# Kernel tuning notes

Hardware: AMD Instinct MI355X
Metric: run time of the kernel (lower is better)

The kernel has to match this reference:

```python
import jax, jax.numpy as jnp
import numpy as np

N_HEADS = 16
SEG = 64
EPS = 1e-6


def _sigma(x):
    # ELU(x) + 1 kernel feature map (strictly positive)
    return jax.nn.elu(x) + 1.0


def setup_inputs() -> dict:
    key = jax.random.key(0)
    kx, kq, kk, kv, ko = jax.random.split(key, 5)
    B, T, D = 4, 4096, 1024
    scale = D ** -0.5
    return {
        "x": jax.random.normal(kx, (B, T, D), dtype=jnp.float32),
        "W_q": jax.random.normal(kq, (D, D), dtype=jnp.float32) * scale,
        "W_k": jax.random.normal(kk, (D, D), dtype=jnp.float32) * scale,
        "W_v": jax.random.normal(kv, (D, D), dtype=jnp.float32) * scale,
        "W_o": jax.random.normal(ko, (D, D), dtype=jnp.float32) * scale,
        "beta_param": jnp.zeros((N_HEADS,), dtype=jnp.float32),
    }


def _infini_attention(x, W_q, W_k, W_v, W_o, beta_param):
    B, T, D = x.shape
    H = N_HEADS
    dk = D // H
    assert T % SEG == 0
    S = T // SEG

    def proj(W):
        # nn.Linear: x @ W.T ; split heads -> (B,H,T,dk) -> (S,B,H,SEG,dk)
        y = (x @ W.T).reshape(B, T, H, dk).transpose(0, 2, 1, 3)
        return y.reshape(B, H, S, SEG, dk).transpose(2, 0, 1, 3, 4)

    Qs, Ks, Vs = proj(W_q), proj(W_k), proj(W_v)

    beta = jax.nn.sigmoid(beta_param).reshape(1, H, 1, 1)
    causal = jnp.triu(jnp.ones((SEG, SEG), dtype=bool), k=1)
    inv_sqrt_dk = 1.0 / jnp.sqrt(jnp.asarray(dk, x.dtype))

    M0 = jnp.zeros((B, H, dk, dk), dtype=x.dtype)
    z0 = jnp.zeros((B, H, dk), dtype=x.dtype)

    def step(carry, qkv):
        M, z = carry
        q, k, v = qkv  # each (B,H,SEG,dk)
        # Eq.4 memory retrieval
        sq = _sigma(q)
        denom_q = jnp.sum(sq * z[:, :, None, :], axis=-1, keepdims=True) + EPS
        A_mem = jnp.matmul(sq, M) / denom_q
        # local causal softmax attention
        scores = jnp.matmul(q, jnp.swapaxes(k, -2, -1)) * inv_sqrt_dk
        scores = jnp.where(causal, -jnp.inf, scores)
        A_dot = jnp.matmul(jax.nn.softmax(scores, axis=-1), v)
        A_s = beta * A_mem + (1.0 - beta) * A_dot
        # Eq.5 delta-rule memory update
        sk = _sigma(k)
        denom_k = jnp.sum(sk * z[:, :, None, :], axis=-1, keepdims=True) + EPS
        V_prev = jnp.matmul(sk, M) / denom_k
        M_new = M + jnp.einsum("bhtk,bhtv->bhkv", sk, v - V_prev)
        z_new = z + jnp.sum(sk, axis=-2)
        return (M_new, z_new), A_s

    (M, z), outs = jax.lax.scan(step, (M0, z0), (Qs, Ks, Vs))
    # outs: (S,B,H,SEG,dk) -> (B,T,D)
    out = outs.transpose(1, 3, 0, 2, 4).reshape(B, S * SEG, H, dk)
    # careful: need segment-major time ordering -> (B, H, T, dk) then (B,T,H,dk)
    out = outs.transpose(1, 2, 0, 3, 4).reshape(B, H, T, dk)
    out = out.transpose(0, 2, 1, 3).reshape(B, T, D)
    out = out @ W_o.T
    return out, M.mean(0), z.mean(0)


def reference(x, W_q, W_k, W_v, W_o, beta_param):
    return _infini_attention(x, W_q, W_k, W_v, W_o, beta_param)
```

## Files before the change

kernel.cpp:

```cpp
#include <hip/hip_runtime.h>

typedef __bf16 bf16_t;
typedef __bf16 bf16x8 __attribute__((ext_vector_type(8)));
typedef __bf16 bf16x4 __attribute__((ext_vector_type(4)));
typedef float  f32x4  __attribute__((ext_vector_type(4)));

__device__ __forceinline__ void gload16(const bf16_t* g, bf16_t* l) {
    __builtin_amdgcn_global_load_lds(
        (const __attribute__((address_space(1))) void*)(g),
        (__attribute__((address_space(3))) void*)(l), 16, 0, 0);
}

__global__ __launch_bounds__(256) void cast_bf16_kernel(const float* __restrict__ in,
                                                        bf16_t* __restrict__ out, int n4) {
    int i = blockIdx.x * 256 + threadIdx.x;
    if (i >= n4) return;
    f32x4 v = *reinterpret_cast<const f32x4*>(in + (size_t)i * 4);
    bf16x4 o;
    o[0] = (bf16_t)v[0]; o[1] = (bf16_t)v[1]; o[2] = (bf16_t)v[2]; o[3] = (bf16_t)v[3];
    *reinterpret_cast<bf16x4*>(out + (size_t)i * 4) = o;
}

__device__ __forceinline__ bf16x8 sigma8(bf16x8 x) {
    bf16x8 o;
#pragma unroll
    for (int j = 0; j < 8; j++) {
        float f = (float)x[j];
        float sg = f > 0.f ? f + 1.f : __expf(f);
        o[j] = (bf16_t)sg;
    }
    return o;
}

template <int OUT_BF16>
__global__ __launch_bounds__(512, 2) void gemm256(const bf16_t* __restrict__ A,
                                                  const bf16_t* __restrict__ Bm,
                                                  void* __restrict__ Cv,
                                                  int M, int N, int K) {
    __shared__ bf16_t As[4][256 * 32];
    __shared__ bf16_t Bs[4][256 * 32];

    int bid = blockIdx.x;
    int xq = bid & 7, jq = bid >> 3;
    int bm = xq * 8 + (jq >> 2), bn = jq & 3;

    int tid = threadIdx.x;
    int w = tid >> 6, lane = tid & 63;
    int wm = w >> 2, wn = w & 3;
    int lr = lane & 15, lk = lane >> 4;

    int srow = lane >> 2;
    int schunk = (lane & 3) ^ (srow & 3);
    const bf16_t* gA0 = A  + (size_t)(bm * 256 + w * 32 + srow) * K + schunk * 8;
    const bf16_t* gA1 = gA0 + (size_t)16 * K;
    const bf16_t* gB0 = Bm + (size_t)(bn * 256 + w * 32 + srow) * K + schunk * 8;
    const bf16_t* gB1 = gB0 + (size_t)16 * K;
    int lO0 = (w * 32) * 32 + lane * 8;
    int lO1 = (w * 32 + 16) * 32 + lane * 8;

    int chunkb = (lk ^ (lr & 3)) << 4;
    int aoff[8], boff[4];
#pragma unroll
    for (int mi = 0; mi < 8; mi++) aoff[mi] = (wm * 128 + mi * 16 + lr) * 64 + chunkb;
#pragma unroll
    for (int ni = 0; ni < 4; ni++) boff[ni] = (wn * 64 + ni * 16 + lr) * 64 + chunkb;

    f32x4 acc[8][4];
#pragma unroll
    for (int mi = 0; mi < 8; mi++)
#pragma unroll
        for (int ni = 0; ni < 4; ni++) acc[mi][ni] = (f32x4){0.f, 0.f, 0.f, 0.f};

    const int NT = K >> 5;

    auto STAGE = [&](int t) {
        int slot = t & 3;
        size_t ko = (size_t)t * 32;
        gload16(gA0 + ko, &As[slot][lO0]);
        gload16(gA1 + ko, &As[slot][lO1]);
        gload16(gB0 + ko, &Bs[slot][lO0]);
        gload16(gB1 + ko, &Bs[slot][lO1]);
    };

    STAGE(0); STAGE(1); STAGE(2);

#pragma unroll 1
    for (int t = 0; t < NT; ++t) {
        int ahead = NT - 1 - t;
        if (ahead >= 2)      asm volatile("s_waitcnt vmcnt(8)" ::: "memory");
        else if (ahead == 1) asm volatile("s_waitcnt vmcnt(4)" ::: "memory");
        else                 asm volatile("s_waitcnt vmcnt(0)" ::: "memory");
        __builtin_amdgcn_sched_barrier(0);
        __builtin_amdgcn_s_barrier();
        __builtin_amdgcn_sched_barrier(0);

        const char* pa = (const char*)(&As[t & 3][0]);
        const char* pb = (const char*)(&Bs[t & 3][0]);
        bf16x8 af[8], bfr[4];
#pragma unroll
        for (int mi = 0; mi < 8; mi++)
            af[mi] = *reinterpret_cast<const bf16x8*>(pa + aoff[mi]);
#pragma unroll
        for (int ni = 0; ni < 4; ni++)
            bfr[ni] = *reinterpret_cast<const bf16x8*>(pb + boff[ni]);

        if (t + 3 < NT) STAGE(t + 3);

        asm volatile("s_waitcnt lgkmcnt(0)" ::: "memory");
        __builtin_amdgcn_sched_barrier(0);
        __builtin_amdgcn_s_setprio(1);
#pragma unroll
        for (int mi = 0; mi < 8; mi++)
#pragma unroll
            for (int ni = 0; ni < 4; ni++)
                acc[mi][ni] = __builtin_amdgcn_mfma_f32_16x16x32_bf16(af[mi], bfr[ni], acc[mi][ni], 0, 0, 0);
        __builtin_amdgcn_s_setprio(0);
    }

    int row0 = bm * 256 + wm * 128 + lk * 4;
    int col0 = bn * 256 + wn * 64 + lr;
#pragma unroll
    for (int mi = 0; mi < 8; mi++)
#pragma unroll
        for (int ni = 0; ni < 4; ni++)
#pragma unroll
            for (int jj = 0; jj < 4; jj++) {
                size_t idx = (size_t)(row0 + mi * 16 + jj) * N + (col0 + ni * 16);
                float v = acc[mi][ni][jj];
                if (OUT_BF16) reinterpret_cast<bf16_t*>(Cv)[idx] = (bf16_t)v;
                else          reinterpret_cast<float*>(Cv)[idx]  = v;
            }
}

__global__ __launch_bounds__(256) void attn_kernel(const bf16_t* __restrict__ Qb,
                                                   bf16_t* __restrict__ Kb,
                                                   bf16_t* __restrict__ Vb,
                                                   bf16_t* __restrict__ skTg,
                                                   float* __restrict__ csum,
                                                   bf16_t* __restrict__ Adot) {
    __shared__ bf16_t kS[64 * 72];
    __shared__ bf16_t vS[64 * 72];
    __shared__ bf16_t skT[64 * 72];
    __shared__ bf16_t vT[64 * 72];
    __shared__ bf16_t pS[64 * 72];
    __shared__ float  scr[64 * 68];

    int u = blockIdx.x;
    int bh = u >> 6, s = u & 63;
    int b = bh >> 4, h = bh & 15;
    int tid = threadIdx.x;
    int w = tid >> 6, lane = tid & 63;
    int lr = lane & 15, lk = lane >> 4;
    int r = tid >> 2, qd = tid & 3, c0 = qd << 4;

    size_t vseg = ((size_t)b * 4096 + s * 64) * 1024 + (size_t)h * 64;
    size_t sb = ((size_t)bh * 64 + s) * 4096;

    {
        bf16x8 k0 = *reinterpret_cast<const bf16x8*>(Kb + vseg + (size_t)r * 1024 + c0);
        bf16x8 k1 = *reinterpret_cast<const bf16x8*>(Kb + vseg + (size_t)r * 1024 + c0 + 8);
        bf16x8 v0 = *reinterpret_cast<const bf16x8*>(Vb + vseg + (size_t)r * 1024 + c0);
        bf16x8 v1 = *reinterpret_cast<const bf16x8*>(Vb + vseg + (size_t)r * 1024 + c0 + 8);
        *reinterpret_cast<bf16x8*>(&kS[r * 72 + c0])     = k0;
        *reinterpret_cast<bf16x8*>(&kS[r * 72 + c0 + 8]) = k1;
        *reinterpret_cast<bf16x8*>(&vS[r * 72 + c0])     = v0;
        *reinterpret_cast<bf16x8*>(&vS[r * 72 + c0 + 8]) = v1;
        bf16x8 s0 = sigma8(k0), s1 = sigma8(k1);
        *reinterpret_cast<bf16x8*>(Kb + vseg + (size_t)r * 1024 + c0)     = s0;
        *reinterpret_cast<bf16x8*>(Kb + vseg + (size_t)r * 1024 + c0 + 8) = s1;
#pragma unroll
        for (int j = 0; j < 8; j++) {
            skT[(c0 + j) * 72 + r]     = s0[j];
            skT[(c0 + 8 + j) * 72 + r] = s1[j];
            vT[(c0 + j) * 72 + r]      = v0[j];
            vT[(c0 + 8 + j) * 72 + r]  = v1[j];
        }
    }
    __syncthreads();

    if (tid < 64) {
        float acc = 0.f;
#pragma unroll 8
        for (int t = 0; t < 64; t++) acc += (float)skT[tid * 72 + t];
        csum[((size_t)bh * 64 + s) * 64 + tid] = acc;
    }
    *reinterpret_cast<bf16x8*>(skTg + sb + (size_t)r * 64 + c0) =
        *reinterpret_cast<const bf16x8*>(&skT[r * 72 + c0]);
    *reinterpret_cast<bf16x8*>(skTg + sb + (size_t)r * 64 + c0 + 8) =
        *reinterpret_cast<const bf16x8*>(&skT[r * 72 + c0 + 8]);
    *reinterpret_cast<bf16x8*>(Vb + vseg + (size_t)r * 1024 + c0) =
        *reinterpret_cast<const bf16x8*>(&vT[r * 72 + c0]);
    *reinterpret_cast<bf16x8*>(Vb + vseg + (size_t)r * 1024 + c0 + 8) =
        *reinterpret_cast<const bf16x8*>(&vT[r * 72 + c0 + 8]);

    {
        bf16x8 aq[2];
#pragma unroll
        for (int ks = 0; ks < 2; ks++)
            aq[ks] = *reinterpret_cast<const bf16x8*>(Qb + vseg + (size_t)(w * 16 + lr) * 1024 + lk * 8 + ks * 32);
        f32x4 sc[4];
#pragma unroll
        for (int ct = 0; ct < 4; ct++) {
            sc[ct] = (f32x4){0.f, 0.f, 0.f, 0.f};
#pragma unroll
            for (int ks = 0; ks < 2; ks++) {
                bf16x8 bfrag = *reinterpret_cast<const bf16x8*>(&kS[(ct * 16 + lr) * 72 + lk * 8 + ks * 32]);
                sc[ct] = __builtin_amdgcn_mfma_f32_16x16x32_bf16(aq[ks], bfrag, sc[ct], 0, 0, 0);
            }
        }
#pragma unroll
        for (int ct = 0; ct < 4; ct++)
#pragma unroll
            for (int j = 0; j < 4; j++)
                scr[(w * 16 + lk * 4 + j) * 68 + ct * 16 + lr] = sc[ct][j] * 0.125f;
    }
    __syncthreads();

    {
        float p[16];
        float mx = -3.4e38f;
        const float* srow_p = &scr[r * 68 + c0];
#pragma unroll
        for (int i = 0; i < 16; i++) {
            int c = c0 + i;
            float v = (c <= r) ? srow_p[i] : -3.4e38f;
            p[i] = v;
            mx = fmaxf(mx, v);
        }
        mx = fmaxf(mx, __shfl_xor(mx, 1));
        mx = fmaxf(mx, __shfl_xor(mx, 2));
        float sum = 0.f;
#pragma unroll
        for (int i = 0; i < 16; i++) {
            int c = c0 + i;
            float e = (c <= r) ? __expf(p[i] - mx) : 0.f;
            p[i] = e;
            sum += e;
        }
        sum += __shfl_xor(sum, 1);
        sum += __shfl_xor(sum, 2);
        float inv = 1.f / sum;
        bf16x8 p0, p1;
#pragma unroll
        for (int j = 0; j < 8; j++) {
            p0[j] = (bf16_t)(p[j] * inv);
            p1[j] = (bf16_t)(p[8 + j] * inv);
        }
        *reinterpret_cast<bf16x8*>(&pS[r * 72 + c0])     = p0;
        *reinterpret_cast<bf16x8*>(&pS[r * 72 + c0 + 8]) = p1;
    }
    __syncthreads();

    {
        f32x4 ad[4];
#pragma unroll
        for (int ct = 0; ct < 4; ct++) {
            ad[ct] = (f32x4){0.f, 0.f, 0.f, 0.f};
#pragma unroll
            for (int ks = 0; ks < 2; ks++) {
                bf16x8 afrag = *reinterpret_cast<const bf16x8*>(&pS[(w * 16 + lr) * 72 + lk * 8 + ks * 32]);
                bf16x8 bfrag = *reinterpret_cast<const bf16x8*>(&vT[(ct * 16 + lr) * 72 + lk * 8 + ks * 32]);
                ad[ct] = __builtin_amdgcn_mfma_f32_16x16x32_bf16(afrag, bfrag, ad[ct], 0, 0, 0);
            }
        }
#pragma unroll
        for (int ct = 0; ct < 4; ct++)
#pragma unroll
            for (int j = 0; j < 4; j++)
                kS[(w * 16 + lk * 4 + j) * 72 + ct * 16 + lr] = (bf16_t)ad[ct][j];
    }
    __syncthreads();
    *reinterpret_cast<bf16x8*>(Adot + sb + (size_t)r * 64 + c0) =
        *reinterpret_cast<const bf16x8*>(&kS[r * 72 + c0]);
    *reinterpret_cast<bf16x8*>(Adot + sb + (size_t)r * 64 + c0 + 8) =
        *reinterpret_cast<const bf16x8*>(&kS[r * 72 + c0 + 8]);
}

__global__ __launch_bounds__(64) void zprefix_kernel(const float* __restrict__ csum,
                                                     float* __restrict__ zx,
                                                     float* __restrict__ zfin) {
    int bh = blockIdx.x;
    int d = threadIdx.x;
    float z = 0.f;
    for (int s = 0; s < 64; s++) {
        size_t o = ((size_t)bh * 64 + s) * 64 + d;
        zx[o] = z;
        z += csum[o];
    }
    zfin[bh * 64 + d] = z;
}

__global__ __launch_bounds__(128) void denom_kernel(const bf16_t* __restrict__ Qb,
                                                    const bf16_t* __restrict__ sK,
                                                    const float* __restrict__ zx,
                                                    float* __restrict__ invq,
                                                    float* __restrict__ invk) {
    __shared__ float zL[64];
    int u = blockIdx.x;
    int bh = u >> 6, s = u & 63;
    int b = bh >> 4, h = bh & 15;
    int tid = threadIdx.x;
    if (tid < 64) zL[tid] = zx[((size_t)bh * 64 + s) * 64 + tid];
    __syncthreads();
    int row = tid & 63;
    bool isq = tid < 64;
    const bf16_t* src = (isq ? Qb : sK) +
                        ((size_t)b * 4096 + s * 64 + row) * 1024 + (size_t)h * 64;
    float acc = 0.f;
#pragma unroll
    for (int blk = 0; blk < 8; blk++) {
        bf16x8 v = *reinterpret_cast<const bf16x8*>(src + blk * 8);
#pragma unroll
        for (int j = 0; j < 8; j++) {
            float f = (float)v[j];
            float sg;
            if (isq) {
                sg = f > 0.f ? f + 1.f : __expf(f);
                sg = (float)(bf16_t)sg;
            } else {
                sg = f;
            }
            acc = __builtin_fmaf(sg, zL[blk * 8 + j], acc);
        }
    }
    float inv = 1.f / (acc + 1e-6f);
    float* dst = isq ? invq : invk;
    dst[((size_t)bh * 64 + s) * 64 + row] = inv;
}

__global__ __launch_bounds__(64, 1) void scan_kernel(const bf16_t* __restrict__ sK,
                                                     const bf16_t* __restrict__ vTg,
                                                     const bf16_t* __restrict__ skTg,
                                                     const float* __restrict__ invk,
                                                     bf16_t* __restrict__ Msnap,
                                                     float* __restrict__ Mfin) {
    __shared__ bf16_t MbL[16 * 72];
    __shared__ bf16_t uTL[16 * 72];
    __shared__ float  ikL[64];

    int blk = blockIdx.x;
    int bh = blk & 63, cq = blk >> 6;
    int c0 = cq << 4;
    int b = bh >> 4, h = bh & 15;
    int lane = threadIdx.x;
    int lr = lane & 15, lk = lane >> 4;
    int vr = lane >> 2, vt0 = (lane & 3) << 4;

    size_t chbase = ((size_t)b * 4096) * 1024 + (size_t)h * 64;
    size_t stbase = (size_t)bh * 64 * 4096;

    auto swz = [](bf16_t* base, int row, int intra) -> bf16_t* {
        return (bf16_t*)((char*)base + row * 144 + (intra ^ ((row & 7) << 4)));
    };

    for (int i = lane; i < 16 * 72; i += 64) MbL[i] = (bf16_t)0.f;
    f32x4 Mreg[4];
#pragma unroll
    for (int rt = 0; rt < 4; rt++) Mreg[rt] = (f32x4){0.f, 0.f, 0.f, 0.f};

    bf16x8 cK[4][2], cT[4][2];
#pragma unroll
    for (int rt = 0; rt < 4; rt++)
#pragma unroll
        for (int ks = 0; ks < 2; ks++) {
            cK[rt][ks] = *reinterpret_cast<const bf16x8*>(
                sK + chbase + (size_t)(rt * 16 + lr) * 1024 + lk * 8 + ks * 32);
            cT[rt][ks] = *reinterpret_cast<const bf16x8*>(
                skTg + stbase + (size_t)(rt * 16 + lr) * 64 + lk * 8 + ks * 32);
        }
    {
        bf16x8 v0 = *reinterpret_cast<const bf16x8*>(vTg + chbase + (size_t)(c0 + vr) * 1024 + vt0);
        bf16x8 v1 = *reinterpret_cast<const bf16x8*>(vTg + chbase + (size_t)(c0 + vr) * 1024 + vt0 + 8);
        *reinterpret_cast<bf16x8*>(swz(uTL, vr, vt0 * 2))      = v0;
        *reinterpret_cast<bf16x8*>(swz(uTL, vr, vt0 * 2 + 16)) = v1;
        ikL[lane] = invk[(size_t)bh * 4096 + lane];
    }

    for (int s = 0; s < 64; s++) {
        bf16x8 nK[4][2], nT[4][2], nv0, nv1;
        float nik = 0.f;
        if (s < 63) {
            size_t vs2 = chbase + (size_t)(s + 1) * 65536;
            size_t sb2 = stbase + (size_t)(s + 1) * 4096;
#pragma unroll
            for (int rt = 0; rt < 4; rt++)
#pragma unroll
                for (int ks = 0; ks < 2; ks++) {
                    nK[rt][ks] = *reinterpret_cast<const bf16x8*>(
                        sK + vs2 + (size_t)(rt * 16 + lr) * 1024 + lk * 8 + ks * 32);
                    nT[rt][ks] = *reinterpret_cast<const bf16x8*>(
                        skTg + sb2 + (size_t)(rt * 16 + lr) * 64 + lk * 8 + ks * 32);
                }
            nv0 = *reinterpret_cast<const bf16x8*>(vTg + vs2 + (size_t)(c0 + vr) * 1024 + vt0);
            nv1 = *reinterpret_cast<const bf16x8*>(vTg + vs2 + (size_t)(c0 + vr) * 1024 + vt0 + 8);
            nik = invk[(size_t)bh * 4096 + (size_t)(s + 1) * 64 + lane];
        }

        bf16x8 mb0 = *reinterpret_cast<const bf16x8*>(swz(MbL, lr, lk * 16));
        bf16x8 mb1 = *reinterpret_cast<const bf16x8*>(swz(MbL, lr, lk * 16 + 64));
        f32x4 Y[4];
#pragma unroll
        for (int rt = 0; rt < 4; rt++) {
            Y[rt] = (f32x4){0.f, 0.f, 0.f, 0.f};
            Y[rt] = __builtin_amdgcn_mfma_f32_16x16x32_bf16(cK[rt][0], mb0, Y[rt], 0, 0, 0);
            Y[rt] = __builtin_amdgcn_mfma_f32_16x16x32_bf16(cK[rt][1], mb1, Y[rt], 0, 0, 0);
        }

#pragma unroll
        for (int rt = 0; rt < 4; rt++) {
            bf16x4 vv = *reinterpret_cast<const bf16x4*>(swz(uTL, lr, rt * 32 + lk * 8));
            bf16x4 uu;
#pragma unroll
            for (int j = 0; j < 4; j++) {
                float ik = ikL[rt * 16 + lk * 4 + j];
                uu[j] = (bf16_t)((float)vv[j] - Y[rt][j] * ik);
            }
            *reinterpret_cast<bf16x4*>(swz(uTL, lr, rt * 32 + lk * 8)) = uu;
        }

        bf16x8 ub0 = *reinterpret_cast<const bf16x8*>(swz(uTL, lr, lk * 16));
        bf16x8 ub1 = *reinterpret_cast<const bf16x8*>(swz(uTL, lr, lk * 16 + 64));
#pragma unroll
        for (int rt = 0; rt < 4; rt++) {
            Mreg[rt] = __builtin_amdgcn_mfma_f32_16x16x32_bf16(cT[rt][0], ub0, Mreg[rt], 0, 0, 0);
            Mreg[rt] = __builtin_amdgcn_mfma_f32_16x16x32_bf16(cT[rt][1], ub1, Mreg[rt], 0, 0, 0);
        }

#pragma unroll
        for (int rt = 0; rt < 4; rt++) {
            bf16x4 mp;
#pragma unroll
            for (int j = 0; j < 4; j++) mp[j] = (bf16_t)Mreg[rt][j];
            *reinterpret_cast<bf16x4*>(swz(MbL, lr, rt * 32 + lk * 8)) = mp;
            if (s < 63)
                *reinterpret_cast<bf16x4*>(
                    Msnap + (((size_t)bh * 64 + s + 1) * 64 + c0 + lr) * 64 + rt * 16 + lk * 4) = mp;
        }

        if (s < 63) {
#pragma unroll
            for (int rt = 0; rt < 4; rt++)
#pragma unroll
                for (int ks = 0; ks < 2; ks++) { cK[rt][ks] = nK[rt][ks]; cT[rt][ks] = nT[rt][ks]; }
            *reinterpret_cast<bf16x8*>(swz(uTL, vr, vt0 * 2))      = nv0;
            *reinterpret_cast<bf16x8*>(swz(uTL, vr, vt0 * 2 + 16)) = nv1;
            ikL[lane] = nik;
        }
    }

#pragma unroll
    for (int rt = 0; rt < 4; rt++)
#pragma unroll
        for (int j = 0; j < 4; j++)
            Mfin[(size_t)bh * 4096 + (size_t)(rt * 16 + lk * 4 + j) * 64 + c0 + lr] = Mreg[rt][j];
}

__global__ __launch_bounds__(256) void combine_kernel(const bf16_t* __restrict__ Qb,
                                                      const bf16_t* __restrict__ Msnap,
                                                      const bf16_t* __restrict__ Adot,
                                                      const float* __restrict__ invq,
                                                      const float* __restrict__ beta_param,
                                                      bf16_t* __restrict__ Op) {
    __shared__ bf16_t oS[64 * 72];
    __shared__ bf16_t adS[64 * 72];
    __shared__ float  iq[64];

    int u = blockIdx.x;
    int bh = u >> 6, s = u & 63;
    int b = bh >> 4, h = bh & 15;
    int tid = threadIdx.x;
    int w = tid >> 6, lane = tid & 63;
    int lr = lane & 15, lk = lane >> 4;
    int r = tid >> 2, c0 = (tid & 3) << 4;

    size_t vseg = ((size_t)b * 4096 + s * 64) * 1024 + (size_t)h * 64;
    size_t sb = ((size_t)bh * 64 + s) * 4096;
    size_t ib = ((size_t)bh * 64 + s) * 64;

    float beta = 1.f / (1.f + __expf(-beta_param[h]));
    float omb = 1.f - beta;

    *reinterpret_cast<bf16x8*>(&adS[r * 72 + c0]) =
        *reinterpret_cast<const bf16x8*>(Adot + sb + (size_t)r * 64 + c0);
    *reinterpret_cast<bf16x8*>(&adS[r * 72 + c0 + 8]) =
        *reinterpret_cast<const bf16x8*>(Adot + sb + (size_t)r * 64 + c0 + 8);
    if (tid < 64) iq[tid] = invq[ib + tid];

    f32x4 Y[4];
#pragma unroll
    for (int ct = 0; ct < 4; ct++) Y[ct] = (f32x4){0.f, 0.f, 0.f, 0.f};
    if (s > 0) {
        bf16x8 aq[2];
#pragma unroll
        for (int ks = 0; ks < 2; ks++)
            aq[ks] = sigma8(*reinterpret_cast<const bf16x8*>(
                Qb + vseg + (size_t)(w * 16 + lr) * 1024 + lk * 8 + ks * 32));
#pragma unroll
        for (int ct = 0; ct < 4; ct++)
#pragma unroll
            for (int ks = 0; ks < 2; ks++) {
                bf16x8 bfrag = *reinterpret_cast<const bf16x8*>(
                    Msnap + sb + (size_t)(ct * 16 + lr) * 64 + lk * 8 + ks * 32);
                Y[ct] = __builtin_amdgcn_mfma_f32_16x16x32_bf16(aq[ks], bfrag, Y[ct], 0, 0, 0);
            }
    }
    __syncthreads();

#pragma unroll
    for (int ct = 0; ct < 4; ct++) {
        int colc = ct * 16 + lr;
#pragma unroll
        for (int j = 0; j < 4; j++) {
            int t = w * 16 + lk * 4 + j;
            float o = beta * (Y[ct][j] * iq[t]) + omb * (float)adS[t * 72 + colc];
            oS[t * 72 + colc] = (bf16_t)o;
        }
    }
    __syncthreads();

    *reinterpret_cast<bf16x8*>(Op + vseg + (size_t)r * 1024 + c0) =
        *reinterpret_cast<const bf16x8*>(&oS[r * 72 + c0]);
    *reinterpret_cast<bf16x8*>(Op + vseg + (size_t)r * 1024 + c0 + 8) =
        *reinterpret_cast<const bf16x8*>(&oS[r * 72 + c0 + 8]);
}

__global__ __launch_bounds__(256) void mean_kernel(const float* __restrict__ Mfin,
                                                   const float* __restrict__ zfin,
                                                   float* __restrict__ out) {
    int idx = blockIdx.x * 256 + threadIdx.x;
    if (idx < 65536) {
        out[16777216 + idx] = 0.25f * (Mfin[idx] + Mfin[idx + 65536] +
                                       Mfin[idx + 131072] + Mfin[idx + 196608]);
    } else if (idx < 66560) {
        int j = idx - 65536;
        out[16842752 + j] = 0.25f * (zfin[j] + zfin[j + 1024] + zfin[j + 2048] + zfin[j + 3072]);
    }
}

extern "C" void kernel_launch(void* const* d_in, const int* in_sizes, int n_in,
                              void* d_out, int out_size, void* d_ws, size_t ws_size,
                              hipStream_t stream) {
    const float* x      = (const float*)d_in[0];
    const float* Wq     = (const float*)d_in[1];
    const float* Wk     = (const float*)d_in[2];
    const float* Wv     = (const float*)d_in[3];
    const float* Wo     = (const float*)d_in[4];
    const float* beta_p = (const float*)d_in[5];
    float* out = (float*)d_out;
    char* ws = (char*)d_ws;

    const size_t NX = 16777216ull;
    const size_t NW = 1048576ull;

    bf16_t* xb   = (bf16_t*)ws;
    bf16_t* Adot = xb;
    bf16_t* Wqb  = (bf16_t*)(ws + 33554432);
    bf16_t* Wkb  = (bf16_t*)(ws + 35651584);
    bf16_t* Wvb  = (bf16_t*)(ws + 37748736);
    bf16_t* Wob  = (bf16_t*)(ws + 39845888);
    bf16_t* Qb   = (bf16_t*)(ws + 41943040);
    bf16_t* Kb   = (bf16_t*)(ws + 75497472);
    bf16_t* Vb   = (bf16_t*)(ws + 109051904);
    bf16_t* skT  = (bf16_t*)(ws + 142606336);
    bf16_t* Op   = (bf16_t*)(ws + 176160768);
    float*  csum = (float*)(ws + 209715200);
    float*  zx   = (float*)(ws + 210763776);
    float*  invq = (float*)(ws + 211812352);
    float*  invk = (float*)(ws + 212860928);
    float*  Mfin = (float*)(ws + 213909504);
    float*  zfin = (float*)(ws + 214958080);
    bf16_t* Msnap = (bf16_t*)d_out;

    cast_bf16_kernel<<<dim3(16384), dim3(256), 0, stream>>>(x, xb, (int)(NX / 4));
    cast_bf16_kernel<<<dim3(1024), dim3(256), 0, stream>>>(Wq, Wqb, (int)(NW / 4));
    cast_bf16_kernel<<<dim3(1024), dim3(256), 0, stream>>>(Wk, Wkb, (int)(NW / 4));
    cast_bf16_kernel<<<dim3(1024), dim3(256), 0, stream>>>(Wv, Wvb, (int)(NW / 4));
    cast_bf16_kernel<<<dim3(1024), dim3(256), 0, stream>>>(Wo, Wob, (int)(NW / 4));

    gemm256<1><<<dim3(256), dim3(512), 0, stream>>>(xb, Wqb, (void*)Qb, 16384, 1024, 1024);
    gemm256<1><<<dim3(256), dim3(512), 0, stream>>>(xb, Wkb, (void*)Kb, 16384, 1024, 1024);
    gemm256<1><<<dim3(256), dim3(512), 0, stream>>>(xb, Wvb, (void*)Vb, 16384, 1024, 1024);

    attn_kernel<<<dim3(4096), dim3(256), 0, stream>>>(Qb, Kb, Vb, skT, csum, Adot);
    zprefix_kernel<<<dim3(64), dim3(64), 0, stream>>>(csum, zx, zfin);
    denom_kernel<<<dim3(4096), dim3(128), 0, stream>>>(Qb, Kb, zx, invq, invk);
    scan_kernel<<<dim3(256), dim3(64), 0, stream>>>(Kb, Vb, skT, invk, Msnap, Mfin);
    combine_kernel<<<dim3(4096), dim3(256), 0, stream>>>(Qb, Msnap, Adot, invq, beta_p, Op);

    gemm256<0><<<dim3(256), dim3(512), 0, stream>>>(Op, Wob, d_out, 16384, 1024, 1024);
    mean_kernel<<<dim3(260), dim3(256), 0, stream>>>(Mfin, zfin, out);
}
```

Before: 347.2 us.

## Replace LDS round-trips in scan kernel with cross-lane shuffles for MFMA B-fragments

The serial per-segment scan kernel used to write the MFMA accumulator layout (M and the delta update) to shared memory and read it back in B-operand layout. It now keeps packed bf16 values in registers and rebuilds the B fragments with __shfl lane permutes and selects. It also loads v and inverse-denominator values straight into the accumulator layout, so no LDS staging is needed. This removes LDS store/load latency from the loop-carried critical path, at the cost of many shuffle instructions and more register pressure.

Measured after the change: 375.2 us. +8.1%, slower.

```diff
diff --git a/kernel.cpp b/kernel.cpp
--- a/kernel.cpp
+++ b/kernel.cpp
@@ -4,6 +4,8 @@
 typedef __bf16 bf16x8 __attribute__((ext_vector_type(8)));
 typedef __bf16 bf16x4 __attribute__((ext_vector_type(4)));
 typedef float  f32x4  __attribute__((ext_vector_type(4)));
+typedef unsigned u32x4 __attribute__((ext_vector_type(4)));
+typedef unsigned u32x2 __attribute__((ext_vector_type(2)));
 
 __device__ __forceinline__ void gload16(const bf16_t* g, bf16_t* l) {
     __builtin_amdgcn_global_load_lds(
@@ -334,33 +336,29 @@
                                                      const float* __restrict__ invk,
                                                      bf16_t* __restrict__ Msnap,
                                                      float* __restrict__ Mfin) {
-    __shared__ bf16_t MbL[16 * 72];
-    __shared__ bf16_t uTL[16 * 72];
-    __shared__ float  ikL[64];
-
     int blk = blockIdx.x;
     int bh = blk & 63, cq = blk >> 6;
     int c0 = cq << 4;
     int b = bh >> 4, h = bh & 15;
     int lane = threadIdx.x;
     int lr = lane & 15, lk = lane >> 4;
-    int vr = lane >> 2, vt0 = (lane & 3) << 4;
+    int hi = lk >> 1;
+    int sel0 = lr + ((lk & 1) << 5);
+    int sel1 = sel0 + 16;
 
     size_t chbase = ((size_t)b * 4096) * 1024 + (size_t)h * 64;
     size_t stbase = (size_t)bh * 64 * 4096;
 
-    auto swz = [](bf16_t* base, int row, int intra) -> bf16_t* {
-        return (bf16_t*)((char*)base + row * 144 + (intra ^ ((row & 7) << 4)));
-    };
-
-    for (int i = lane; i < 16 * 72; i += 64) MbL[i] = (bf16_t)0.f;
     f32x4 Mreg[4];
 #pragma unroll
     for (int rt = 0; rt < 4; rt++) Mreg[rt] = (f32x4){0.f, 0.f, 0.f, 0.f};
+    unsigned pM0[2] = {0u, 0u}, pM1[2] = {0u, 0u}, pM2[2] = {0u, 0u}, pM3[2] = {0u, 0u};
 
     bf16x8 cK[4][2], cT[4][2];
-#pragma unroll
-    for (int rt = 0; rt < 4; rt++)
+    bf16x4 vv[4];
+    f32x4  ik[4];
+#pragma unroll
+    for (int rt = 0; rt < 4; rt++) {
 #pragma unroll
         for (int ks = 0; ks < 2; ks++) {
             cK[rt][ks] = *reinterpret_cast<const bf16x8*>(
@@ -368,22 +366,41 @@
             cT[rt][ks] = *reinterpret_cast<const bf16x8*>(
                 skTg + stbase + (size_t)(rt * 16 + lr) * 64 + lk * 8 + ks * 32);
         }
-    {
-        bf16x8 v0 = *reinterpret_cast<const bf16x8*>(vTg + chbase + (size_t)(c0 + vr) * 1024 + vt0);
-        bf16x8 v1 = *reinterpret_cast<const bf16x8*>(vTg + chbase + (size_t)(c0 + vr) * 1024 + vt0 + 8);
-        *reinterpret_cast<bf16x8*>(swz(uTL, vr, vt0 * 2))      = v0;
-        *reinterpret_cast<bf16x8*>(swz(uTL, vr, vt0 * 2 + 16)) = v1;
-        ikL[lane] = invk[(size_t)bh * 4096 + lane];
-    }
-
+        vv[rt] = *reinterpret_cast<const bf16x4*>(
+            vTg + chbase + (size_t)(c0 + lr) * 1024 + rt * 16 + lk * 4);
+        ik[rt] = *reinterpret_cast<const f32x4*>(
+            invk + (size_t)bh * 4096 + rt * 16 + lk * 4);
+    }
+
+#define BFRAG_FROM_PACKS(OUT0, OUT1, Q0, Q1, Q2, Q3)                                   \
+    {                                                                                  \
+        unsigned a0_0 = __shfl((int)Q0[0], sel0), a0_1 = __shfl((int)Q0[1], sel0);     \
+        unsigned b0_0 = __shfl((int)Q0[0], sel1), b0_1 = __shfl((int)Q0[1], sel1);     \
+        unsigned a1_0 = __shfl((int)Q1[0], sel0), a1_1 = __shfl((int)Q1[1], sel0);     \
+        unsigned b1_0 = __shfl((int)Q1[0], sel1), b1_1 = __shfl((int)Q1[1], sel1);     \
+        unsigned a2_0 = __shfl((int)Q2[0], sel0), a2_1 = __shfl((int)Q2[1], sel0);     \
+        unsigned b2_0 = __shfl((int)Q2[0], sel1), b2_1 = __shfl((int)Q2[1], sel1);     \
+        unsigned a3_0 = __shfl((int)Q3[0], sel0), a3_1 = __shfl((int)Q3[1], sel0);     \
+        unsigned b3_0 = __shfl((int)Q3[0], sel1), b3_1 = __shfl((int)Q3[1], sel1);     \
+        u32x4 t0, t1;                                                                  \
+        t0[0] = hi ? a1_0 : a0_0;  t0[1] = hi ? a1_1 : a0_1;                           \
+        t0[2] = hi ? b1_0 : b0_0;  t0[3] = hi ? b1_1 : b0_1;                           \
+        t1[0] = hi ? a3_0 : a2_0;  t1[1] = hi ? a3_1 : a2_1;                           \
+        t1[2] = hi ? b3_0 : b2_0;  t1[3] = hi ? b3_1 : b2_1;                           \
+        OUT0 = __builtin_bit_cast(bf16x8, t0);                                         \
+        OUT1 = __builtin_bit_cast(bf16x8, t1);                                         \
+    }
+
+#pragma unroll 1
     for (int s = 0; s < 64; s++) {
-        bf16x8 nK[4][2], nT[4][2], nv0, nv1;
-        float nik = 0.f;
+        bf16x8 nK[4][2], nT[4][2];
+        bf16x4 nv[4];
+        f32x4  nik[4];
         if (s < 63) {
             size_t vs2 = chbase + (size_t)(s + 1) * 65536;
             size_t sb2 = stbase + (size_t)(s + 1) * 4096;
 #pragma unroll
-            for (int rt = 0; rt < 4; rt++)
+            for (int rt = 0; rt < 4; rt++) {
 #pragma unroll
                 for (int ks = 0; ks < 2; ks++) {
                     nK[rt][ks] = *reinterpret_cast<const bf16x8*>(
@@ -391,13 +408,16 @@
                     nT[rt][ks] = *reinterpret_cast<const bf16x8*>(
                         skTg + sb2 + (size_t)(rt * 16 + lr) * 64 + lk * 8 + ks * 32);
                 }
-            nv0 = *reinterpret_cast<const bf16x8*>(vTg + vs2 + (size_t)(c0 + vr) * 1024 + vt0);
-            nv1 = *reinterpret_cast<const bf16x8*>(vTg + vs2 + (size_t)(c0 + vr) * 1024 + vt0 + 8);
-            nik = invk[(size_t)bh * 4096 + (size_t)(s + 1) * 64 + lane];
-        }
-
-        bf16x8 mb0 = *reinterpret_cast<const bf16x8*>(swz(MbL, lr, lk * 16));
-        bf16x8 mb1 = *reinterpret_cast<const bf16x8*>(swz(MbL, lr, lk * 16 + 64));
+                nv[rt] = *reinterpret_cast<const bf16x4*>(
+                    vTg + vs2 + (size_t)(c0 + lr) * 1024 + rt * 16 + lk * 4);
+                nik[rt] = *reinterpret_cast<const f32x4*>(
+                    invk + (size_t)bh * 4096 + (size_t)(s + 1) * 64 + rt * 16 + lk * 4);
+            }
+        }
+
+        bf16x8 mb0, mb1;
+        BFRAG_FROM_PACKS(mb0, mb1, pM0, pM1, pM2, pM3);
+
         f32x4 Y[4];
 #pragma unroll
         for (int rt = 0; rt < 4; rt++) {
@@ -406,47 +426,62 @@
             Y[rt] = __builtin_amdgcn_mfma_f32_16x16x32_bf16(cK[rt][1], mb1, Y[rt], 0, 0, 0);
         }
 
-#pragma unroll
-        for (int rt = 0; rt < 4; rt++) {
-            bf16x4 vv = *reinterpret_cast<const bf16x4*>(swz(uTL, lr, rt * 32 + lk * 8));
-            bf16x4 uu;
-#pragma unroll
-            for (int j = 0; j < 4; j++) {
-                float ik = ikL[rt * 16 + lk * 4 + j];
-                uu[j] = (bf16_t)((float)vv[j] - Y[rt][j] * ik);
-            }
-            *reinterpret_cast<bf16x4*>(swz(uTL, lr, rt * 32 + lk * 8)) = uu;
-        }
-
-        bf16x8 ub0 = *reinterpret_cast<const bf16x8*>(swz(uTL, lr, lk * 16));
-        bf16x8 ub1 = *reinterpret_cast<const bf16x8*>(swz(uTL, lr, lk * 16 + 64));
+        unsigned pu0[2], pu1[2], pu2[2], pu3[2];
+        {
+            bf16x4 uu[4];
+#pragma unroll
+            for (int rt = 0; rt < 4; rt++) {
+#pragma unroll
+                for (int j = 0; j < 4; j++)
+                    uu[rt][j] = (bf16_t)((float)vv[rt][j] - Y[rt][j] * ik[rt][j]);
+            }
+            u32x2 q;
+            q = __builtin_bit_cast(u32x2, uu[0]); pu0[0] = q[0]; pu0[1] = q[1];
+            q = __builtin_bit_cast(u32x2, uu[1]); pu1[0] = q[0]; pu1[1] = q[1];
+            q = __builtin_bit_cast(u32x2, uu[2]); pu2[0] = q[0]; pu2[1] = q[1];
+            q = __builtin_bit_cast(u32x2, uu[3]); pu3[0] = q[0]; pu3[1] = q[1];
+        }
+
+        bf16x8 ub0, ub1;
+        BFRAG_FROM_PACKS(ub0, ub1, pu0, pu1, pu2, pu3);
+
 #pragma unroll
         for (int rt = 0; rt < 4; rt++) {
             Mreg[rt] = __builtin_amdgcn_mfma_f32_16x16x32_bf16(cT[rt][0], ub0, Mreg[rt], 0, 0, 0);
             Mreg[rt] = __builtin_amdgcn_mfma_f32_16x16x32_bf16(cT[rt][1], ub1, Mreg[rt], 0, 0, 0);
         }
 
-#pragma unroll
-        for (int rt = 0; rt < 4; rt++) {
-            bf16x4 mp;
-#pragma unroll
-            for (int j = 0; j < 4; j++) mp[j] = (bf16_t)Mreg[rt][j];
-            *reinterpret_cast<bf16x4*>(swz(MbL, lr, rt * 32 + lk * 8)) = mp;
-            if (s < 63)
-                *reinterpret_cast<bf16x4*>(
-                    Msnap + (((size_t)bh * 64 + s + 1) * 64 + c0 + lr) * 64 + rt * 16 + lk * 4) = mp;
+        {
+            bf16x4 mp[4];
+#pragma unroll
+            for (int rt = 0; rt < 4; rt++) {
+#pragma unroll
+                for (int j = 0; j < 4; j++) mp[rt][j] = (bf16_t)Mreg[rt][j];
+            }
+            u32x2 q;
+            q = __builtin_bit_cast(u32x2, mp[0]); pM0[0] = q[0]; pM0[1] = q[1];
+            q = __builtin_bit_cast(u32x2, mp[1]); pM1[0] = q[0]; pM1[1] = q[1];
+            q = __builtin_bit_cast(u32x2, mp[2]); pM2[0] = q[0]; pM2[1] = q[1];
+            q = __builtin_bit_cast(u32x2, mp[3]); pM3[0] = q[0]; pM3[1] = q[1];
+            if (s < 63) {
+#pragma unroll
+                for (int rt = 0; rt < 4; rt++)
+                    *reinterpret_cast<bf16x4*>(
+                        Msnap + (((size_t)bh * 64 + s + 1) * 64 + c0 + lr) * 64 + rt * 16 + lk * 4) = mp[rt];
+            }
         }
 
         if (s < 63) {
 #pragma unroll
-            for (int rt = 0; rt < 4; rt++)
+            for (int rt = 0; rt < 4; rt++) {
 #pragma unroll
                 for (int ks = 0; ks < 2; ks++) { cK[rt][ks] = nK[rt][ks]; cT[rt][ks] = nT[rt][ks]; }
-            *reinterpret_cast<bf16x8*>(swz(uTL, vr, vt0 * 2))      = nv0;
-            *reinterpret_cast<bf16x8*>(swz(uTL, vr, vt0 * 2 + 16)) = nv1;
-            ikL[lane] = nik;
-        }
-    }
+                vv[rt] = nv[rt];
+                ik[rt] = nik[rt];
+            }
+        }
+    }
+#undef BFRAG_FROM_PACKS
 
 #pragma unroll
     for (int rt = 0; rt < 4; rt++)
```
